# Performance work log

Measured on AMD Instinct MI355X. Metric: run time of the kernel, lower is better.

The kernel has to match this reference:

```python
import jax, jax.numpy as jnp
import numpy as np

B, S, K, D, H, COND, MR = 4, 1024, 1024, 1024, 16, 1024, 4
HD = D // H  # 64
INV_SQRT_HD = 1.0 / float(np.sqrt(HD))
GELU_C = 0.7978845608028654  # sqrt(2/pi)


def _make_rope(seqlen):
    pos = jnp.arange(seqlen, dtype=jnp.float32)
    inv = 1.0 / (10000.0 ** (jnp.arange(0, HD // 2, dtype=jnp.float32) * 2.0 / HD))
    ang = pos[:, None] * inv[None, :]                     # [S, HD/2]
    cos = jnp.concatenate([jnp.cos(ang), jnp.cos(ang)], -1)  # [S, HD]
    sin = jnp.concatenate([jnp.sin(ang), jnp.sin(ang)], -1)
    return cos[None, :, None, :], sin[None, :, None, :]   # [1,S,1,HD]


def setup_inputs():
    key = jax.random.key(0)
    ks = jax.random.split(key, 14)
    rn = lambda k, shape, s=0.02: jax.random.normal(k, shape, jnp.float32) * s
    cos_q, sin_q = _make_rope(S)
    cos_k, sin_k = _make_rope(K)
    ada_b = jnp.zeros((6 * D,), jnp.float32)
    ada_b = ada_b.at[2 * D:3 * D].set(0.5).at[5 * D:6 * D].set(0.5)  # gate_msa, gate_mlp init
    return {
        "q_x": jax.random.normal(ks[0], (B, S, D), jnp.float32),
        "kv_x": jax.random.normal(ks[1], (B, K, D), jnp.float32),
        "t_cond": jax.random.normal(ks[2], (B, COND), jnp.float32),
        "cos_q": cos_q, "sin_q": sin_q, "cos_k": cos_k, "sin_k": sin_k,
        "group_idxs": jax.random.randint(ks[3], (B, S), 0, 4, jnp.int32),
        "query_enabled": jax.random.randint(ks[4], (B, S), 0, 2, jnp.int32).astype(bool),
        "qn_w": jnp.ones((D,), jnp.float32),
        "kvn_w": jnp.ones((D,), jnp.float32),
        "n2_w": jnp.ones((D,), jnp.float32),
        "Wq": rn(ks[5], (D, D)), "Wkv": rn(ks[6], (D, 2 * D)), "Wo": rn(ks[7], (D, D)),
        "W1": rn(ks[8], (D, MR * D)), "b1": jnp.zeros((MR * D,), jnp.float32),
        "W2": rn(ks[9], (MR * D, D)), "b2": jnp.zeros((D,), jnp.float32),
        "adaW": rn(ks[10], (COND, 6 * D)), "adab": ada_b,
    }


def layer_norm(x, w):
    mu = jnp.mean(x, -1, keepdims=True)
    var = jnp.var(x, -1, keepdims=True)
    return (x - mu) * jax.lax.rsqrt(var + 1e-5) * w


def rope(x, cos, sin):
    # x: [B,S,H,HD]; cos/sin: [1,S,1,HD]; rotate_half convention
    x1, x2 = jnp.split(x, 2, axis=-1)
    return x * cos + jnp.concatenate([-x2, x1], -1) * sin


def gelu_tanh(x):
    return 0.5 * x * (1.0 + jnp.tanh(GELU_C * (x + 0.044715 * x * x * x)))


def reference(q_x, kv_x, t_cond, cos_q, sin_q, cos_k, sin_k, group_idxs, query_enabled,
              qn_w, kvn_w, n2_w, Wq, Wkv, Wo, W1, b1, W2, b2, adaW, adab):
    # adaLN modulation (inference: dropout disabled -> bias_dropout_add_scale = scale*x + residual)
    mod = (t_cond @ adaW + adab)[:, None, :]               # [B,1,6D]
    sh_msa, sc_msa, g_msa, sh_mlp, sc_mlp, g_mlp = jnp.split(mod, 6, axis=-1)

    qn = layer_norm(q_x, qn_w)
    kvn = layer_norm(kv_x, kvn_w)
    qn = qn * (1.0 + sc_msa) + sh_msa                      # modulate_fused

    q = (qn @ Wq).reshape(B, S, H, HD)
    kv = (kvn @ Wkv).reshape(B, K, 2, H, HD)
    k, v = kv[:, :, 0], kv[:, :, 1]
    q = rope(q, cos_q, sin_q)
    k = rope(k, cos_k, sin_k)

    # group cross-attn mask: attend only where groups differ
    attend = group_idxs[:, :, None] != group_idxs[:, None, :]  # [B,S,K]
    scores = jnp.einsum('bqhd,bkhd->bhqk', q, k) * INV_SQRT_HD
    scores = jnp.where(attend[:, None, :, :], scores, -1e9)
    p = jax.nn.softmax(scores, axis=-1)
    attn = jnp.einsum('bhqk,bkhd->bqhd', p, v).reshape(B, S, D)

    x = g_msa * (attn @ Wo) + q_x                          # fused bias-dropout-add-scale (inference)
    gate = query_enabled[..., None].astype(x.dtype)
    x = x * gate + q_x * (1.0 - gate)                      # gated_update

    x_mid = x
    h = layer_norm(x, n2_w) * (1.0 + sc_mlp) + sh_mlp
    h = gelu_tanh(h @ W1 + b1) @ W2 + b2
    x = g_mlp * h + x_mid
    x = x * gate + x_mid * (1.0 - gate)
    return x
```

## Files before the change

kernel.cpp:

```cpp
#include <hip/hip_runtime.h>
#include <hip/hip_bf16.h>
#include <math.h>

typedef __bf16 bf16_t;
typedef __attribute__((ext_vector_type(8))) __bf16 bf16x8;
typedef __attribute__((ext_vector_type(4))) __bf16 bf16x4;
typedef __attribute__((ext_vector_type(4))) float f32x4;

__global__ __launch_bounds__(256) void compact_kernel(
    const int* __restrict__ qen, int* __restrict__ idx, int* __restrict__ McPtr)
{
  __shared__ int cnts[256];
  int t = threadIdx.x;
  int flags[16], c = 0;
#pragma unroll
  for (int i = 0; i < 16; ++i) {
    flags[i] = qen[t * 16 + i] != 0;
    c += flags[i];
  }
  cnts[t] = c;
  __syncthreads();
  for (int off = 1; off < 256; off <<= 1) {
    int v = cnts[t];
    if (t >= off) v += cnts[t - off];
    __syncthreads();
    cnts[t] = v;
    __syncthreads();
  }
  int p = cnts[t] - c;
  int total = cnts[255];
#pragma unroll
  for (int i = 0; i < 16; ++i)
    if (flags[i]) idx[p++] = t * 16 + i;
  if (t == 0) *McPtr = total;
  for (int j = total + t; j < 4096; j += 256) idx[j] = 0;
}

__global__ __launch_bounds__(256) void copy_disabled_kernel(
    const int* __restrict__ qen, const float* __restrict__ qx,
    float* __restrict__ out)
{
  int row = blockIdx.x;
  if (qen[row]) return;
  int tid = threadIdx.x;
  ((float4*)(out + (size_t)row * 1024))[tid] =
      ((const float4*)(qx + (size_t)row * 1024))[tid];
}

__global__ __launch_bounds__(256) void mod_init_kernel(
    const float* __restrict__ adab, float* __restrict__ mod)
{
  int i = blockIdx.x * 256 + threadIdx.x;
  mod[i] = adab[i % 6144];
}

__global__ __launch_bounds__(256) void mod_partial_kernel(
    const float* __restrict__ tc, const float* __restrict__ adaW,
    float* __restrict__ mod)
{
  __shared__ float st[4][128];
  int tid = threadIdx.x, z = blockIdx.y;
  for (int i = tid; i < 512; i += 256)
    st[i >> 7][i & 127] = tc[(i >> 7) * 1024 + z * 128 + (i & 127)];
  __syncthreads();
  int col = blockIdx.x * 256 + tid;
  float a0 = 0.f, a1 = 0.f, a2 = 0.f, a3 = 0.f;
  for (int k = 0; k < 128; ++k) {
    float wv = adaW[(size_t)(z * 128 + k) * 6144 + col];
    a0 = fmaf(st[0][k], wv, a0);
    a1 = fmaf(st[1][k], wv, a1);
    a2 = fmaf(st[2][k], wv, a2);
    a3 = fmaf(st[3][k], wv, a3);
  }
  atomicAdd(&mod[col], a0);
  atomicAdd(&mod[6144 + col], a1);
  atomicAdd(&mod[2 * 6144 + col], a2);
  atomicAdd(&mod[3 * 6144 + col], a3);
}

__global__ __launch_bounds__(256) void transpose_all(
    const float* __restrict__ Wq, const float* __restrict__ Wkv,
    const float* __restrict__ Wo, const float* __restrict__ W1,
    const float* __restrict__ W2,
    bf16_t* __restrict__ oWq, bf16_t* __restrict__ oWkv,
    bf16_t* __restrict__ oWo, bf16_t* __restrict__ oW1,
    bf16_t* __restrict__ oW2)
{
  __shared__ float tile[32][33];
  int bid = blockIdx.x;
  const float* in; bf16_t* out; int R, C, gx, local;
  if (bid < 1024)      { in = Wq;  out = oWq;  R = 1024; C = 1024; gx = 32;  local = bid; }
  else if (bid < 3072) { in = Wkv; out = oWkv; R = 1024; C = 2048; gx = 64;  local = bid - 1024; }
  else if (bid < 4096) { in = Wo;  out = oWo;  R = 1024; C = 1024; gx = 32;  local = bid - 3072; }
  else if (bid < 8192) { in = W1;  out = oW1;  R = 1024; C = 4096; gx = 128; local = bid - 4096; }
  else                 { in = W2;  out = oW2;  R = 4096; C = 1024; gx = 32;  local = bid - 8192; }
  int c0 = (local % gx) * 32, r0 = (local / gx) * 32;
  int tx = threadIdx.x, ty = threadIdx.y;
#pragma unroll
  for (int i = 0; i < 4; ++i)
    tile[ty + i * 8][tx] = in[(size_t)(r0 + ty + i * 8) * C + c0 + tx];
  __syncthreads();
#pragma unroll
  for (int i = 0; i < 4; ++i)
    out[(size_t)(c0 + ty + i * 8) * R + r0 + tx] = (bf16_t)tile[tx][ty + i * 8];
}

__global__ __launch_bounds__(256) void ln_both_kernel(
    const float* __restrict__ qx, const float* __restrict__ kvx,
    const float* __restrict__ qnw, const float* __restrict__ kvnw,
    const float* __restrict__ mod,
    bf16_t* __restrict__ qn_out, bf16_t* __restrict__ kvn_out)
{
  int rowg = blockIdx.x;
  bool isQ = rowg < 4096;
  int row = isQ ? rowg : rowg - 4096;
  int b = row >> 10;
  int tid = threadIdx.x;
  const float* x = (isQ ? qx : kvx) + (size_t)row * 1024;
  const float* wgt = isQ ? qnw : kvnw;
  bf16_t* outp = (isQ ? qn_out : kvn_out) + (size_t)row * 1024;

  float4 v = ((const float4*)x)[tid];
  float s = v.x + v.y + v.z + v.w;
  float s2 = v.x * v.x + v.y * v.y + v.z * v.z + v.w * v.w;
#pragma unroll
  for (int off = 32; off > 0; off >>= 1) {
    s += __shfl_down(s, off, 64);
    s2 += __shfl_down(s2, off, 64);
  }
  __shared__ float ps[4], ps2[4];
  if ((tid & 63) == 0) { ps[tid >> 6] = s; ps2[tid >> 6] = s2; }
  __syncthreads();
  float mu = (ps[0] + ps[1] + ps[2] + ps[3]) * (1.0f / 1024.0f);
  float var = (ps2[0] + ps2[1] + ps2[2] + ps2[3]) * (1.0f / 1024.0f) - mu * mu;
  float rs = rsqrtf(var + 1e-5f);
  float xv[4] = {v.x, v.y, v.z, v.w};
#pragma unroll
  for (int i = 0; i < 4; ++i) {
    int col = tid * 4 + i;
    float n = (xv[i] - mu) * rs * wgt[col];
    if (isQ)
      n = n * (1.0f + mod[b * 6144 + 1024 + col]) + mod[b * 6144 + col];
    outp[col] = (bf16_t)n;
  }
}

__global__ __launch_bounds__(256) void reduce_q_rope_kernel(
    const bf16_t* __restrict__ P0, const bf16_t* __restrict__ P1,
    const float* __restrict__ cosq, const float* __restrict__ sinq,
    bf16_t* __restrict__ qr)
{
  int t = blockIdx.x * 256 + threadIdx.x;
  int hd = t & 31;
  int h = (t >> 5) & 15;
  int s = (t >> 9) & 1023;
  int b = t >> 19;
  size_t base = ((size_t)(b * 1024 + s)) * 1024 + h * 64 + hd;
  float v1 = (float)P0[base] + (float)P1[base];
  float v2 = (float)P0[base + 32] + (float)P1[base + 32];
  float c1 = cosq[s * 64 + hd], s1 = sinq[s * 64 + hd];
  float c2 = cosq[s * 64 + hd + 32], s2 = sinq[s * 64 + hd + 32];
  float o1 = (v1 * c1 - v2 * s1) * 0.125f;
  float o2 = (v2 * c2 + v1 * s2) * 0.125f;
  size_t ob = ((size_t)(b * 16 + h) * 1024 + s) * 64 + hd;
  qr[ob] = (bf16_t)o1;
  qr[ob + 32] = (bf16_t)o2;
}

__global__ __launch_bounds__(256) void reduce_kv_kernel(
    const bf16_t* __restrict__ P0, const bf16_t* __restrict__ P1,
    const float* __restrict__ cosk, const float* __restrict__ sink,
    bf16_t* __restrict__ kr, bf16_t* __restrict__ vt)
{
  __shared__ float ks[64][65];
  __shared__ float vs[64][65];
  int bh = blockIdx.x;
  int b = bh >> 4, h = bh & 15;
  int n0 = blockIdx.y * 64;
  int tid = threadIdx.x;
#pragma unroll
  for (int it = 0; it < 16; ++it) {
    int linear = tid + it * 256;
    int nl = linear >> 6, hd = linear & 63;
    size_t gi = ((size_t)(b * 1024 + n0 + nl)) * 2048 + h * 64 + hd;
    ks[nl][hd] = (float)P0[gi] + (float)P1[gi];
    vs[hd][nl] = (float)P0[gi + 1024] + (float)P1[gi + 1024];
  }
  __syncthreads();
#pragma unroll
  for (int it = 0; it < 16; ++it) {
    int linear = tid + it * 256;
    int nl = linear >> 6, hd = linear & 63;
    float kv = ks[nl][hd];
    float pv = ks[nl][hd ^ 32];
    float c = cosk[(n0 + nl) * 64 + hd], sn = sink[(n0 + nl) * 64 + hd];
    float o = (hd < 32) ? (kv * c - pv * sn) : (kv * c + pv * sn);
    kr[((size_t)bh * 1024 + n0 + nl) * 64 + hd] = (bf16_t)o;
    vt[((size_t)bh * 64 + nl) * 1024 + n0 + hd] = (bf16_t)vs[nl][hd];
  }
}

__global__ __launch_bounds__(256, 4) void attn_kernel(
    const bf16_t* __restrict__ qr, const bf16_t* __restrict__ kr,
    const bf16_t* __restrict__ vt, const int* __restrict__ grp,
    bf16_t* __restrict__ Op, float* __restrict__ lbuf)
{
  __shared__ bf16_t Ks[64 * 68];
  __shared__ bf16_t Vs[64 * 68];
  __shared__ bf16_t Ps[128 * 68];
  __shared__ int gk[64];
  const int bh = blockIdx.x;
  const int b = bh >> 4, h = bh & 15;
  const int qBase = blockIdx.y * 128;
  const int z = blockIdx.z;
  const int tid = threadIdx.x, lane = tid & 63, w = tid >> 6;
  const int l15 = lane & 15, l4 = lane >> 4;
  const f32x4 zero = {0.f, 0.f, 0.f, 0.f};

  bf16x8 qA0[2], qA1[2];
  int gqr[2][4];
#pragma unroll
  for (int s = 0; s < 2; ++s) {
    int row = qBase + w * 32 + s * 16;
    const bf16_t* qp = qr + ((size_t)bh * 1024 + row + l15) * 64;
    qA0[s] = *(const bf16x8*)(qp + l4 * 8);
    qA1[s] = *(const bf16x8*)(qp + 32 + l4 * 8);
#pragma unroll
    for (int r = 0; r < 4; ++r) gqr[s][r] = grp[b * 1024 + row + l4 * 4 + r];
  }

  f32x4 oacc[2][4];
  float rsum[2][4];
#pragma unroll
  for (int s = 0; s < 2; ++s)
#pragma unroll
    for (int i = 0; i < 4; ++i) { oacc[s][i] = zero; rsum[s][i] = 0.f; }

  for (int kt = z * 8; kt < z * 8 + 8; ++kt) {
    __syncthreads();
#pragma unroll
    for (int i = 0; i < 2; ++i) {
      int c = tid * 2 + i;
      int r = c >> 3, cc = (c & 7) * 8;
      *(bf16x8*)(Ks + r * 68 + cc) =
          *(const bf16x8*)(kr + ((size_t)bh * 1024 + kt * 64 + r) * 64 + cc);
      *(bf16x8*)(Vs + r * 68 + cc) =
          *(const bf16x8*)(vt + ((size_t)bh * 64 + r) * 1024 + kt * 64 + cc);
    }
    if (tid < 64) gk[tid] = grp[b * 1024 + kt * 64 + tid];
    __syncthreads();

    int gkv[4];
    bf16x8 kf0[4], kf1[4];
#pragma unroll
    for (int nt = 0; nt < 4; ++nt) {
      gkv[nt] = gk[nt * 16 + l15];
      kf0[nt] = *(const bf16x8*)(Ks + (nt * 16 + l15) * 68 + l4 * 8);
      kf1[nt] = *(const bf16x8*)(Ks + (nt * 16 + l15) * 68 + 32 + l4 * 8);
    }

#pragma unroll
    for (int s = 0; s < 2; ++s) {
      f32x4 sacc[4];
#pragma unroll
      for (int nt = 0; nt < 4; ++nt) sacc[nt] = zero;
#pragma unroll
      for (int nt = 0; nt < 4; ++nt) {
        sacc[nt] = __builtin_amdgcn_mfma_f32_16x16x32_bf16(qA0[s], kf0[nt], sacc[nt], 0, 0, 0);
        sacc[nt] = __builtin_amdgcn_mfma_f32_16x16x32_bf16(qA1[s], kf1[nt], sacc[nt], 0, 0, 0);
      }
#pragma unroll
      for (int r = 0; r < 4; ++r) {
        int gq = gqr[s][r];
        float acc = 0.f;
#pragma unroll
        for (int nt = 0; nt < 4; ++nt) {
          float sv = sacc[nt][r] + ((gq == gkv[nt]) ? -60.f : 0.f);
          float p = __expf(sv);
          acc += p;
          Ps[(w * 32 + s * 16 + l4 * 4 + r) * 68 + nt * 16 + l15] = (bf16_t)p;
        }
        rsum[s][r] += acc;
      }
    }
#pragma unroll
    for (int s = 0; s < 2; ++s) {
      const bf16_t* pp = Ps + (w * 32 + s * 16 + l15) * 68;
      bf16x8 pf0 = *(const bf16x8*)(pp + l4 * 8);
      bf16x8 pf1 = *(const bf16x8*)(pp + 32 + l4 * 8);
#pragma unroll
      for (int nt = 0; nt < 4; ++nt) {
        bf16x8 vf0 = *(const bf16x8*)(Vs + (nt * 16 + l15) * 68 + l4 * 8);
        bf16x8 vf1 = *(const bf16x8*)(Vs + (nt * 16 + l15) * 68 + 32 + l4 * 8);
        oacc[s][nt] = __builtin_amdgcn_mfma_f32_16x16x32_bf16(pf0, vf0, oacc[s][nt], 0, 0, 0);
        oacc[s][nt] = __builtin_amdgcn_mfma_f32_16x16x32_bf16(pf1, vf1, oacc[s][nt], 0, 0, 0);
      }
    }
  }

#pragma unroll
  for (int s = 0; s < 2; ++s)
#pragma unroll
    for (int r = 0; r < 4; ++r) {
      float t = rsum[s][r];
      t += __shfl_xor(t, 1, 64);
      t += __shfl_xor(t, 2, 64);
      t += __shfl_xor(t, 4, 64);
      t += __shfl_xor(t, 8, 64);
      int row = qBase + w * 32 + s * 16 + l4 * 4 + r;
      if (l15 == 0) lbuf[z * 65536 + bh * 1024 + row] = t;
#pragma unroll
      for (int nt = 0; nt < 4; ++nt)
        Op[(size_t)z * 4194304 + ((size_t)(b * 1024 + row)) * 1024 + h * 64 +
           nt * 16 + l15] = (bf16_t)oacc[s][nt][r];
    }
}

__global__ __launch_bounds__(256) void attn_reduce_kernel(
    const bf16_t* __restrict__ Op, const float* __restrict__ lbuf,
    bf16_t* __restrict__ attn_o)
{
  int row = blockIdx.x;
  int b = row >> 10, s = row & 1023;
  int tid = threadIdx.x;
  int h = tid >> 4;
  float l0 = lbuf[(b * 16 + h) * 1024 + s];
  float l1 = lbuf[65536 + (b * 16 + h) * 1024 + s];
  float inv = 1.f / (l0 + l1);
  size_t ro = (size_t)row * 1024 + tid * 4;
  bf16x4 o0 = *(const bf16x4*)(Op + ro);
  bf16x4 o1 = *(const bf16x4*)(Op + 4194304 + ro);
  bf16x4 o;
#pragma unroll
  for (int i = 0; i < 4; ++i)
    o[i] = (bf16_t)(((float)o0[i] + (float)o1[i]) * inv);
  *(bf16x4*)(attn_o + ro) = o;
}

__device__ __forceinline__ void stage16(const bf16_t* gp, bf16_t* lp) {
  __builtin_amdgcn_global_load_lds(
      (__attribute__((address_space(1))) void*)gp,
      (__attribute__((address_space(3))) void*)lp, 16, 0, 0);
}

__global__ __launch_bounds__(256, 2) void gemm_qkv(
    const bf16_t* __restrict__ qn, const bf16_t* __restrict__ WqT,
    const bf16_t* __restrict__ kvn, const bf16_t* __restrict__ WkvT,
    bf16_t* __restrict__ scr)
{
  __shared__ bf16_t sA[128 * 64];
  __shared__ bf16_t sB[128 * 64];
  const int tid = threadIdx.x;
  const int lane = tid & 63, w = tid >> 6;
  const int wr = w >> 1, wc = w & 1;
  const int z = blockIdx.z;

  const int L = blockIdx.y * 24 + blockIdx.x;
  const int xcd = L & 7, id2 = L >> 3;
  const int tileY = (xcd & 3) * 8 + (id2 % 8);
  const int tileX = (xcd >> 2) * 12 + (id2 / 8);
  const int rowBase = tileY * 128;

  const bf16_t* A;
  const bf16_t* Bt;
  bf16_t* Cb;
  int N, colBase;
  size_t zOff;
  if (tileX < 8) {
    A = qn; Bt = WqT; N = 1024; colBase = tileX * 128;
    Cb = scr; zOff = (size_t)z * 4194304;
  } else {
    A = kvn; Bt = WkvT; N = 2048; colBase = (tileX - 8) * 128;
    Cb = scr + 8388608; zOff = (size_t)z * 8388608;
  }

  const int l15 = lane & 15, l4 = lane >> 4;
  const int srow = lane >> 3;
  const int sg = lane & 7;
  const int scol = (sg ^ srow) * 8;
  const int rl = l15 & 7;
  const int g0 = (l4 ^ rl) * 8;
  const int g1 = ((4 + l4) ^ rl) * 8;

  const f32x4 zero = {0.f, 0.f, 0.f, 0.f};
  f32x4 acc[4][4];
#pragma unroll
  for (int i = 0; i < 4; ++i)
#pragma unroll
    for (int j = 0; j < 4; ++j) acc[i][j] = zero;

  const bf16_t* aBase = A + (size_t)(rowBase + w * 32 + srow) * 1024 + scol;
  const bf16_t* bBase = Bt + (size_t)(colBase + w * 32 + srow) * 1024 + scol;

  const int kStart = z * 512;
  for (int k0 = kStart; k0 < kStart + 512; k0 += 64) {
    __syncthreads();
#pragma unroll
    for (int i = 0; i < 4; ++i) {
      stage16(aBase + (size_t)i * 8 * 1024 + k0, sA + (w * 32 + i * 8) * 64);
      stage16(bBase + (size_t)i * 8 * 1024 + k0, sB + (w * 32 + i * 8) * 64);
    }
    __syncthreads();
    bf16x8 af[4], bfr[4];
#pragma unroll
    for (int mt = 0; mt < 4; ++mt)
      af[mt] = *(const bf16x8*)(sA + (wr * 64 + mt * 16 + l15) * 64 + g0);
#pragma unroll
    for (int nt = 0; nt < 4; ++nt)
      bfr[nt] = *(const bf16x8*)(sB + (wc * 64 + nt * 16 + l15) * 64 + g0);
#pragma unroll
    for (int mt = 0; mt < 4; ++mt)
#pragma unroll
      for (int nt = 0; nt < 4; ++nt)
        acc[mt][nt] = __builtin_amdgcn_mfma_f32_16x16x32_bf16(af[mt], bfr[nt],
                                                              acc[mt][nt], 0, 0, 0);
#pragma unroll
    for (int mt = 0; mt < 4; ++mt)
      af[mt] = *(const bf16x8*)(sA + (wr * 64 + mt * 16 + l15) * 64 + g1);
#pragma unroll
    for (int nt = 0; nt < 4; ++nt)
      bfr[nt] = *(const bf16x8*)(sB + (wc * 64 + nt * 16 + l15) * 64 + g1);
#pragma unroll
    for (int mt = 0; mt < 4; ++mt)
#pragma unroll
      for (int nt = 0; nt < 4; ++nt)
        acc[mt][nt] = __builtin_amdgcn_mfma_f32_16x16x32_bf16(af[mt], bfr[nt],
                                                              acc[mt][nt], 0, 0, 0);
  }

#pragma unroll
  for (int mt = 0; mt < 4; ++mt)
#pragma unroll
    for (int nt = 0; nt < 4; ++nt) {
      int col = colBase + wc * 64 + nt * 16 + l15;
#pragma unroll
      for (int r = 0; r < 4; ++r) {
        int rr = rowBase + wr * 64 + mt * 16 + l4 * 4 + r;
        Cb[zOff + (size_t)rr * N + col] = (bf16_t)acc[mt][nt][r];
      }
    }
}

template <int EPI, int GATHER>
__global__ __launch_bounds__(256, 2) void gemm64_c(
    const bf16_t* __restrict__ A, const bf16_t* __restrict__ Bt,
    int N, int Kd, int kChunk, bf16_t* __restrict__ Cb,
    const float* __restrict__ bias,
    const int* __restrict__ idxG, const int* __restrict__ McPtr)
{
  __shared__ bf16_t sA[64 * 64];
  __shared__ bf16_t sB[128 * 64];
  const int Mc = *McPtr;
  const int gx = gridDim.x;
  const int L = blockIdx.y * gx + blockIdx.x;
  const int xcd = L & 7, id2 = L >> 3;
  const int tileY = (id2 / gx) * 8 + xcd;
  const int tileX = id2 % gx;
  const int rowBase = tileY * 64;
  if (rowBase >= Mc) return;
  const int colBase = tileX * 128;

  const int tid = threadIdx.x;
  const int lane = tid & 63, w = tid >> 6;
  const int wr = w >> 1, wc = w & 1;
  const int l15 = lane & 15, l4 = lane >> 4;
  const int srow = lane >> 3;
  const int sg = lane & 7;
  const int scol = (sg ^ srow) * 8;
  const int rl = l15 & 7;
  const int g0 = (l4 ^ rl) * 8;
  const int g1 = ((4 + l4) ^ rl) * 8;

  const f32x4 zero = {0.f, 0.f, 0.f, 0.f};
  f32x4 acc[2][4];
#pragma unroll
  for (int i = 0; i < 2; ++i)
#pragma unroll
    for (int j = 0; j < 4; ++j) acc[i][j] = zero;

  const bf16_t* aB[2];
#pragma unroll
  for (int i = 0; i < 2; ++i) {
    int rowc = rowBase + w * 16 + i * 8 + srow;
    int arow = GATHER ? idxG[rowc] : rowc;
    aB[i] = A + (size_t)arow * Kd + scol;
  }
  const bf16_t* bBase = Bt + (size_t)(colBase + w * 32 + srow) * Kd + scol;

  const int kStart = blockIdx.z * kChunk;
  for (int k0 = kStart; k0 < kStart + kChunk; k0 += 64) {
    __syncthreads();
#pragma unroll
    for (int i = 0; i < 2; ++i)
      stage16(aB[i] + k0, sA + (w * 16 + i * 8) * 64);
#pragma unroll
    for (int i = 0; i < 4; ++i)
      stage16(bBase + (size_t)i * 8 * Kd + k0, sB + (w * 32 + i * 8) * 64);
    __syncthreads();
    bf16x8 af[2], bfr[4];
#pragma unroll
    for (int mt = 0; mt < 2; ++mt)
      af[mt] = *(const bf16x8*)(sA + (wr * 32 + mt * 16 + l15) * 64 + g0);
#pragma unroll
    for (int nt = 0; nt < 4; ++nt)
      bfr[nt] = *(const bf16x8*)(sB + (wc * 64 + nt * 16 + l15) * 64 + g0);
#pragma unroll
    for (int mt = 0; mt < 2; ++mt)
#pragma unroll
      for (int nt = 0; nt < 4; ++nt)
        acc[mt][nt] = __builtin_amdgcn_mfma_f32_16x16x32_bf16(af[mt], bfr[nt],
                                                              acc[mt][nt], 0, 0, 0);
#pragma unroll
    for (int mt = 0; mt < 2; ++mt)
      af[mt] = *(const bf16x8*)(sA + (wr * 32 + mt * 16 + l15) * 64 + g1);
#pragma unroll
    for (int nt = 0; nt < 4; ++nt)
      bfr[nt] = *(const bf16x8*)(sB + (wc * 64 + nt * 16 + l15) * 64 + g1);
#pragma unroll
    for (int mt = 0; mt < 2; ++mt)
#pragma unroll
      for (int nt = 0; nt < 4; ++nt)
        acc[mt][nt] = __builtin_amdgcn_mfma_f32_16x16x32_bf16(af[mt], bfr[nt],
                                                              acc[mt][nt], 0, 0, 0);
  }

  const size_t zOff = (size_t)blockIdx.z * 4096 * N;
#pragma unroll
  for (int mt = 0; mt < 2; ++mt)
#pragma unroll
    for (int nt = 0; nt < 4; ++nt) {
      int col = colBase + wc * 64 + nt * 16 + l15;
#pragma unroll
      for (int r = 0; r < 4; ++r) {
        int rr = rowBase + wr * 32 + mt * 16 + l4 * 4 + r;
        float v = acc[mt][nt][r];
        if constexpr (EPI == 1) {
          float t = v + bias[col];
          float zz = 0.7978845608028654f * (t + 0.044715f * t * t * t);
          float e = __expf(2.f * zz);
          float g = 0.5f * t * (2.f - 2.f / (e + 1.f));
          Cb[(size_t)rr * N + col] = (bf16_t)g;
        } else {
          Cb[zOff + (size_t)rr * N + col] = (bf16_t)v;
        }
      }
    }
}

__global__ __launch_bounds__(256) void ln2_fused_kernel(
    const bf16_t* __restrict__ P, const float* __restrict__ qx,
    const float* __restrict__ n2w, const float* __restrict__ mod,
    const int* __restrict__ idxG, const int* __restrict__ McPtr,
    float* __restrict__ xbufc, bf16_t* __restrict__ xnc)
{
  int rowc = blockIdx.x;
  if (rowc >= *McPtr) return;
  int rr = idxG[rowc];
  int b = rr >> 10;
  int tid = threadIdx.x;
  size_t rc = (size_t)rowc * 1024 + tid * 4;
  bf16x4 p0 = *(const bf16x4*)(P + rc);
  bf16x4 p1 = *(const bf16x4*)(P + 4194304 + rc);
  bf16x4 p2 = *(const bf16x4*)(P + 2 * 4194304 + rc);
  bf16x4 p3 = *(const bf16x4*)(P + 3 * 4194304 + rc);
  float4 res = ((const float4*)(qx + (size_t)rr * 1024))[tid];
  float4 g = ((const float4*)(mod + b * 6144 + 2048))[tid];
  float4 x;
  x.x = fmaf(g.x, (float)p0[0] + (float)p1[0] + (float)p2[0] + (float)p3[0], res.x);
  x.y = fmaf(g.y, (float)p0[1] + (float)p1[1] + (float)p2[1] + (float)p3[1], res.y);
  x.z = fmaf(g.z, (float)p0[2] + (float)p1[2] + (float)p2[2] + (float)p3[2], res.z);
  x.w = fmaf(g.w, (float)p0[3] + (float)p1[3] + (float)p2[3] + (float)p3[3], res.w);
  *(float4*)(xbufc + rc) = x;

  float s = x.x + x.y + x.z + x.w;
  float s2 = x.x * x.x + x.y * x.y + x.z * x.z + x.w * x.w;
#pragma unroll
  for (int off = 32; off > 0; off >>= 1) {
    s += __shfl_down(s, off, 64);
    s2 += __shfl_down(s2, off, 64);
  }
  __shared__ float ps[4], ps2[4];
  if ((tid & 63) == 0) { ps[tid >> 6] = s; ps2[tid >> 6] = s2; }
  __syncthreads();
  float mu = (ps[0] + ps[1] + ps[2] + ps[3]) * (1.0f / 1024.0f);
  float var = (ps2[0] + ps2[1] + ps2[2] + ps2[3]) * (1.0f / 1024.0f) - mu * mu;
  float rs = rsqrtf(var + 1e-5f);
  float4 sc = ((const float4*)(mod + b * 6144 + 4096))[tid];
  float4 sh = ((const float4*)(mod + b * 6144 + 3072))[tid];
  float4 wv = ((const float4*)n2w)[tid];
  float xv[4] = {x.x, x.y, x.z, x.w};
  float scv[4] = {sc.x, sc.y, sc.z, sc.w};
  float shv[4] = {sh.x, sh.y, sh.z, sh.w};
  float wvv[4] = {wv.x, wv.y, wv.z, wv.w};
#pragma unroll
  for (int i = 0; i < 4; ++i) {
    float n = (xv[i] - mu) * rs * wvv[i];
    n = n * (1.0f + scv[i]) + shv[i];
    xnc[(size_t)rowc * 1024 + tid * 4 + i] = (bf16_t)n;
  }
}

__global__ __launch_bounds__(256) void final_reduce_kernel(
    const bf16_t* __restrict__ P, const float* __restrict__ b2,
    const float* __restrict__ mod, const int* __restrict__ idxG,
    const int* __restrict__ McPtr, const float* __restrict__ xbufc,
    float* __restrict__ out)
{
  int rowc = blockIdx.x;
  if (rowc >= *McPtr) return;
  int rr = idxG[rowc];
  int b = rr >> 10;
  int tid = threadIdx.x;
  size_t rc = (size_t)rowc * 1024 + tid * 4;
  bf16x4 p0 = *(const bf16x4*)(P + rc);
  bf16x4 p1 = *(const bf16x4*)(P + 4194304 + rc);
  bf16x4 p2 = *(const bf16x4*)(P + 2 * 4194304 + rc);
  bf16x4 p3 = *(const bf16x4*)(P + 3 * 4194304 + rc);
  float4 bb = ((const float4*)b2)[tid];
  float4 xm = *(const float4*)(xbufc + rc);
  float4 g = ((const float4*)(mod + b * 6144 + 5120))[tid];
  float v0 = (float)p0[0] + (float)p1[0] + (float)p2[0] + (float)p3[0] + bb.x;
  float v1 = (float)p0[1] + (float)p1[1] + (float)p2[1] + (float)p3[1] + bb.y;
  float v2 = (float)p0[2] + (float)p1[2] + (float)p2[2] + (float)p3[2] + bb.z;
  float v3 = (float)p0[3] + (float)p1[3] + (float)p2[3] + (float)p3[3] + bb.w;
  float4 o;
  o.x = fmaf(g.x, v0, xm.x);
  o.y = fmaf(g.y, v1, xm.y);
  o.z = fmaf(g.z, v2, xm.z);
  o.w = fmaf(g.w, v3, xm.w);
  *(float4*)(out + (size_t)rr * 1024 + tid * 4) = o;
}

extern "C" void kernel_launch(void* const* d_in, const int* in_sizes, int n_in,
                              void* d_out, int out_size, void* d_ws, size_t ws_size,
                              hipStream_t stream)
{
  const float* q_x    = (const float*)d_in[0];
  const float* kv_x   = (const float*)d_in[1];
  const float* t_cond = (const float*)d_in[2];
  const float* cos_q  = (const float*)d_in[3];
  const float* sin_q  = (const float*)d_in[4];
  const float* cos_k  = (const float*)d_in[5];
  const float* sin_k  = (const float*)d_in[6];
  const int*   grp    = (const int*)d_in[7];
  const int*   qen    = (const int*)d_in[8];
  const float* qn_w   = (const float*)d_in[9];
  const float* kvn_w  = (const float*)d_in[10];
  const float* n2_w   = (const float*)d_in[11];
  const float* Wq     = (const float*)d_in[12];
  const float* Wkv    = (const float*)d_in[13];
  const float* Wo     = (const float*)d_in[14];
  const float* W1     = (const float*)d_in[15];
  const float* b1     = (const float*)d_in[16];
  const float* W2     = (const float*)d_in[17];
  const float* b2     = (const float*)d_in[18];
  const float* adaW   = (const float*)d_in[19];
  const float* adab   = (const float*)d_in[20];
  float* out = (float*)d_out;

  char* ws = (char*)d_ws;
  const size_t MB = 1ull << 20;
  float*  mod    = (float*)(ws + 0);
  int*    idxL   = (int*)(ws + 98304);
  int*    McPtr  = (int*)(ws + 98304 + 16384);
  char*   wbase  = ws + 131072;
  bf16_t* Wq_t   = (bf16_t*)(wbase);
  bf16_t* Wkv_t  = (bf16_t*)(wbase + 2 * MB);
  bf16_t* Wo_t   = (bf16_t*)(wbase + 6 * MB);
  bf16_t* W1_t   = (bf16_t*)(wbase + 8 * MB);
  bf16_t* W2_t   = (bf16_t*)(wbase + 16 * MB);
  bf16_t* qn_mod = (bf16_t*)(wbase + 24 * MB);
  bf16_t* kvn    = (bf16_t*)(wbase + 32 * MB);
  bf16_t* q_r    = (bf16_t*)(wbase + 40 * MB);
  bf16_t* k_r    = (bf16_t*)(wbase + 48 * MB);
  bf16_t* v_t    = (bf16_t*)(wbase + 56 * MB);
  bf16_t* h1     = (bf16_t*)(wbase + 64 * MB);
  bf16_t* scr    = (bf16_t*)(wbase + 96 * MB);
  bf16_t* xn_c   = qn_mod;
  bf16_t* attn_o = kvn;
  float*  xbuf_c = (float*)q_r;
  bf16_t* attn_p = scr;
  float*  lbuf   = (float*)(scr + 8388608);

  compact_kernel<<<1, 256, 0, stream>>>(qen, idxL, McPtr);
  copy_disabled_kernel<<<4096, 256, 0, stream>>>(qen, q_x, out);
  mod_init_kernel<<<96, 256, 0, stream>>>(adab, mod);
  mod_partial_kernel<<<dim3(24, 8), 256, 0, stream>>>(t_cond, adaW, mod);
  transpose_all<<<12288, dim3(32, 8), 0, stream>>>(Wq, Wkv, Wo, W1, W2,
                                                   Wq_t, Wkv_t, Wo_t, W1_t, W2_t);
  ln_both_kernel<<<8192, 256, 0, stream>>>(q_x, kv_x, qn_w, kvn_w, mod,
                                           qn_mod, kvn);
  gemm_qkv<<<dim3(24, 32, 2), 256, 0, stream>>>(qn_mod, Wq_t, kvn, Wkv_t, scr);
  reduce_q_rope_kernel<<<8192, 256, 0, stream>>>(scr, scr + 4194304, cos_q, sin_q, q_r);
  reduce_kv_kernel<<<dim3(64, 16), 256, 0, stream>>>(scr + 8388608, scr + 16777216,
                                                     cos_k, sin_k, k_r, v_t);
  attn_kernel<<<dim3(64, 8, 2), 256, 0, stream>>>(q_r, k_r, v_t, grp, attn_p, lbuf);
  attn_reduce_kernel<<<4096, 256, 0, stream>>>(attn_p, lbuf, attn_o);
  gemm64_c<4, 1><<<dim3(8, 64, 4), 256, 0, stream>>>(attn_o, Wo_t, 1024, 1024, 256,
                                                     scr, nullptr, idxL, McPtr);
  ln2_fused_kernel<<<4096, 256, 0, stream>>>(scr, q_x, n2_w, mod, idxL, McPtr,
                                             xbuf_c, xn_c);
  gemm64_c<1, 0><<<dim3(32, 64, 1), 256, 0, stream>>>(xn_c, W1_t, 4096, 1024, 1024,
                                                      h1, b1, idxL, McPtr);
  gemm64_c<4, 0><<<dim3(8, 64, 4), 256, 0, stream>>>(h1, W2_t, 1024, 4096, 1024,
                                                     scr, nullptr, idxL, McPtr);
  final_reduce_kernel<<<4096, 256, 0, stream>>>(scr, b2, mod, idxL, McPtr, xbuf_c, out);
}
```

Before: 405.6 us.

## Drop split-K attention and normalize inside the attention kernel

Attention now processes all 16 key tiles in a single block, with 64 query rows per block (16 per wave) instead of 128 rows split across two key halves. The softmax normalization happens in-kernel, so the partial-output buffers and the separate attn_reduce kernel are gone. This removes the partial write and read traffic plus one launch. In exchange each block reloads K and V for only 64 queries, which doubles K/V staging traffic per query, and the loop over keys is twice as long.

```diff
diff --git a/kernel.cpp b/kernel.cpp
--- a/kernel.cpp
+++ b/kernel.cpp
@@ -203,40 +203,33 @@
 __global__ __launch_bounds__(256, 4) void attn_kernel(
     const bf16_t* __restrict__ qr, const bf16_t* __restrict__ kr,
     const bf16_t* __restrict__ vt, const int* __restrict__ grp,
-    bf16_t* __restrict__ Op, float* __restrict__ lbuf)
+    bf16_t* __restrict__ outp)
 {
   __shared__ bf16_t Ks[64 * 68];
   __shared__ bf16_t Vs[64 * 68];
-  __shared__ bf16_t Ps[128 * 68];
+  __shared__ bf16_t Ps[64 * 68];
   __shared__ int gk[64];
   const int bh = blockIdx.x;
   const int b = bh >> 4, h = bh & 15;
-  const int qBase = blockIdx.y * 128;
-  const int z = blockIdx.z;
+  const int qBase = blockIdx.y * 64;
   const int tid = threadIdx.x, lane = tid & 63, w = tid >> 6;
   const int l15 = lane & 15, l4 = lane >> 4;
   const f32x4 zero = {0.f, 0.f, 0.f, 0.f};
 
-  bf16x8 qA0[2], qA1[2];
-  int gqr[2][4];
-#pragma unroll
-  for (int s = 0; s < 2; ++s) {
-    int row = qBase + w * 32 + s * 16;
-    const bf16_t* qp = qr + ((size_t)bh * 1024 + row + l15) * 64;
-    qA0[s] = *(const bf16x8*)(qp + l4 * 8);
-    qA1[s] = *(const bf16x8*)(qp + 32 + l4 * 8);
-#pragma unroll
-    for (int r = 0; r < 4; ++r) gqr[s][r] = grp[b * 1024 + row + l4 * 4 + r];
-  }
-
-  f32x4 oacc[2][4];
-  float rsum[2][4];
-#pragma unroll
-  for (int s = 0; s < 2; ++s)
-#pragma unroll
-    for (int i = 0; i < 4; ++i) { oacc[s][i] = zero; rsum[s][i] = 0.f; }
-
-  for (int kt = z * 8; kt < z * 8 + 8; ++kt) {
+  const int qrow = qBase + w * 16;
+  const bf16_t* qp = qr + ((size_t)bh * 1024 + qrow + l15) * 64;
+  bf16x8 qA0 = *(const bf16x8*)(qp + l4 * 8);
+  bf16x8 qA1 = *(const bf16x8*)(qp + 32 + l4 * 8);
+  int gqr[4];
+#pragma unroll
+  for (int r = 0; r < 4; ++r) gqr[r] = grp[b * 1024 + qrow + l4 * 4 + r];
+
+  f32x4 oacc[4];
+  float rsum[4];
+#pragma unroll
+  for (int i = 0; i < 4; ++i) { oacc[i] = zero; rsum[i] = 0.f; }
+
+  for (int kt = 0; kt < 16; ++kt) {
     __syncthreads();
 #pragma unroll
     for (int i = 0; i < 2; ++i) {
@@ -250,91 +243,55 @@
     if (tid < 64) gk[tid] = grp[b * 1024 + kt * 64 + tid];
     __syncthreads();
 
-    int gkv[4];
-    bf16x8 kf0[4], kf1[4];
+    f32x4 sacc[4];
+#pragma unroll
+    for (int nt = 0; nt < 4; ++nt) sacc[nt] = zero;
 #pragma unroll
     for (int nt = 0; nt < 4; ++nt) {
-      gkv[nt] = gk[nt * 16 + l15];
-      kf0[nt] = *(const bf16x8*)(Ks + (nt * 16 + l15) * 68 + l4 * 8);
-      kf1[nt] = *(const bf16x8*)(Ks + (nt * 16 + l15) * 68 + 32 + l4 * 8);
+      bf16x8 kf0 = *(const bf16x8*)(Ks + (nt * 16 + l15) * 68 + l4 * 8);
+      bf16x8 kf1 = *(const bf16x8*)(Ks + (nt * 16 + l15) * 68 + 32 + l4 * 8);
+      sacc[nt] = __builtin_amdgcn_mfma_f32_16x16x32_bf16(qA0, kf0, sacc[nt], 0, 0, 0);
+      sacc[nt] = __builtin_amdgcn_mfma_f32_16x16x32_bf16(qA1, kf1, sacc[nt], 0, 0, 0);
     }
-
-#pragma unroll
-    for (int s = 0; s < 2; ++s) {
-      f32x4 sacc[4];
-#pragma unroll
-      for (int nt = 0; nt < 4; ++nt) sacc[nt] = zero;
+#pragma unroll
+    for (int r = 0; r < 4; ++r) {
+      int gq = gqr[r];
+      float acc = 0.f;
 #pragma unroll
       for (int nt = 0; nt < 4; ++nt) {
-        sacc[nt] = __builtin_amdgcn_mfma_f32_16x16x32_bf16(qA0[s], kf0[nt], sacc[nt], 0, 0, 0);
-        sacc[nt] = __builtin_amdgcn_mfma_f32_16x16x32_bf16(qA1[s], kf1[nt], sacc[nt], 0, 0, 0);
+        float sv = sacc[nt][r] + ((gq == gk[nt * 16 + l15]) ? -60.f : 0.f);
+        float p = __expf(sv);
+        acc += p;
+        Ps[(w * 16 + l4 * 4 + r) * 68 + nt * 16 + l15] = (bf16_t)p;
       }
-#pragma unroll
-      for (int r = 0; r < 4; ++r) {
-        int gq = gqr[s][r];
-        float acc = 0.f;
-#pragma unroll
-        for (int nt = 0; nt < 4; ++nt) {
-          float sv = sacc[nt][r] + ((gq == gkv[nt]) ? -60.f : 0.f);
-          float p = __expf(sv);
-          acc += p;
-          Ps[(w * 32 + s * 16 + l4 * 4 + r) * 68 + nt * 16 + l15] = (bf16_t)p;
-        }
-        rsum[s][r] += acc;
-      }
+      rsum[r] += acc;
     }
-#pragma unroll
-    for (int s = 0; s < 2; ++s) {
-      const bf16_t* pp = Ps + (w * 32 + s * 16 + l15) * 68;
-      bf16x8 pf0 = *(const bf16x8*)(pp + l4 * 8);
-      bf16x8 pf1 = *(const bf16x8*)(pp + 32 + l4 * 8);
-#pragma unroll
-      for (int nt = 0; nt < 4; ++nt) {
-        bf16x8 vf0 = *(const bf16x8*)(Vs + (nt * 16 + l15) * 68 + l4 * 8);
-        bf16x8 vf1 = *(const bf16x8*)(Vs + (nt * 16 + l15) * 68 + 32 + l4 * 8);
-        oacc[s][nt] = __builtin_amdgcn_mfma_f32_16x16x32_bf16(pf0, vf0, oacc[s][nt], 0, 0, 0);
-        oacc[s][nt] = __builtin_amdgcn_mfma_f32_16x16x32_bf16(pf1, vf1, oacc[s][nt], 0, 0, 0);
-      }
+    const bf16_t* pp = Ps + (w * 16 + l15) * 68;
+    bf16x8 pf0 = *(const bf16x8*)(pp + l4 * 8);
+    bf16x8 pf1 = *(const bf16x8*)(pp + 32 + l4 * 8);
+#pragma unroll
+    for (int nt = 0; nt < 4; ++nt) {
+      bf16x8 vf0 = *(const bf16x8*)(Vs + (nt * 16 + l15) * 68 + l4 * 8);
+      bf16x8 vf1 = *(const bf16x8*)(Vs + (nt * 16 + l15) * 68 + 32 + l4 * 8);
+      oacc[nt] = __builtin_amdgcn_mfma_f32_16x16x32_bf16(pf0, vf0, oacc[nt], 0, 0, 0);
+      oacc[nt] = __builtin_amdgcn_mfma_f32_16x16x32_bf16(pf1, vf1, oacc[nt], 0, 0, 0);
     }
   }
 
 #pragma unroll
-  for (int s = 0; s < 2; ++s)
-#pragma unroll
-    for (int r = 0; r < 4; ++r) {
-      float t = rsum[s][r];
-      t += __shfl_xor(t, 1, 64);
-      t += __shfl_xor(t, 2, 64);
-      t += __shfl_xor(t, 4, 64);
-      t += __shfl_xor(t, 8, 64);
-      int row = qBase + w * 32 + s * 16 + l4 * 4 + r;
-      if (l15 == 0) lbuf[z * 65536 + bh * 1024 + row] = t;
-#pragma unroll
-      for (int nt = 0; nt < 4; ++nt)
-        Op[(size_t)z * 4194304 + ((size_t)(b * 1024 + row)) * 1024 + h * 64 +
-           nt * 16 + l15] = (bf16_t)oacc[s][nt][r];
-    }
-}
-
-__global__ __launch_bounds__(256) void attn_reduce_kernel(
-    const bf16_t* __restrict__ Op, const float* __restrict__ lbuf,
-    bf16_t* __restrict__ attn_o)
-{
-  int row = blockIdx.x;
-  int b = row >> 10, s = row & 1023;
-  int tid = threadIdx.x;
-  int h = tid >> 4;
-  float l0 = lbuf[(b * 16 + h) * 1024 + s];
-  float l1 = lbuf[65536 + (b * 16 + h) * 1024 + s];
-  float inv = 1.f / (l0 + l1);
-  size_t ro = (size_t)row * 1024 + tid * 4;
-  bf16x4 o0 = *(const bf16x4*)(Op + ro);
-  bf16x4 o1 = *(const bf16x4*)(Op + 4194304 + ro);
-  bf16x4 o;
-#pragma unroll
-  for (int i = 0; i < 4; ++i)
-    o[i] = (bf16_t)(((float)o0[i] + (float)o1[i]) * inv);
-  *(bf16x4*)(attn_o + ro) = o;
+  for (int r = 0; r < 4; ++r) {
+    float t = rsum[r];
+    t += __shfl_xor(t, 1, 64);
+    t += __shfl_xor(t, 2, 64);
+    t += __shfl_xor(t, 4, 64);
+    t += __shfl_xor(t, 8, 64);
+    float inv = 1.f / t;
+    int srow = qBase + w * 16 + l4 * 4 + r;
+#pragma unroll
+    for (int nt = 0; nt < 4; ++nt)
+      outp[((size_t)(b * 1024 + srow)) * 1024 + h * 64 + nt * 16 + l15] =
+          (bf16_t)(oacc[nt][r] * inv);
+  }
 }
 
 __device__ __forceinline__ void stage16(const bf16_t* gp, bf16_t* lp) {
@@ -679,8 +636,6 @@
   bf16_t* xn_c   = qn_mod;
   bf16_t* attn_o = kvn;
   float*  xbuf_c = (float*)q_r;
-  bf16_t* attn_p = scr;
-  float*  lbuf   = (float*)(scr + 8388608);
 
   compact_kernel<<<1, 256, 0, stream>>>(qen, idxL, McPtr);
   copy_disabled_kernel<<<4096, 256, 0, stream>>>(qen, q_x, out);
@@ -694,8 +649,7 @@
   reduce_q_rope_kernel<<<8192, 256, 0, stream>>>(scr, scr + 4194304, cos_q, sin_q, q_r);
   reduce_kv_kernel<<<dim3(64, 16), 256, 0, stream>>>(scr + 8388608, scr + 16777216,
                                                      cos_k, sin_k, k_r, v_t);
-  attn_kernel<<<dim3(64, 8, 2), 256, 0, stream>>>(q_r, k_r, v_t, grp, attn_p, lbuf);
-  attn_reduce_kernel<<<4096, 256, 0, stream>>>(attn_p, lbuf, attn_o);
+  attn_kernel<<<dim3(64, 16), 256, 0, stream>>>(q_r, k_r, v_t, grp, attn_o);
   gemm64_c<4, 1><<<dim3(8, 64, 4), 256, 0, stream>>>(attn_o, Wo_t, 1024, 1024, 256,
                                                      scr, nullptr, idxL, McPtr);
   ln2_fused_kernel<<<4096, 256, 0, stream>>>(scr, q_x, n2_w, mod, idxL, McPtr,
```

Result: no change. 411.8 us (+1.5%).
